# Kernel tuning notes

Hardware: AMD Instinct MI355X
Metric: run time of the kernel (lower is better)

Reference implementation:

```python
import jax, jax.numpy as jnp
import numpy as np

EMB = 2048
HD = 64            # head_dim
NH = 32            # n_heads
NKV = 8            # n_kv_groups
GS = NH // NKV     # group_size = 4
WIN = 128          # sliding_window
LAYER_IDX = 0      # even -> sliding-window mask active
ROPE_BASE = 10000.0
MAX_SEQ = 4096
YARN_ORIG = 1024.0
YARN_SCALE = 4.0
YARN_BETA_FAST = 32.0
YARN_BETA_SLOW = 1.0


def _rope_tables():
    # YaRN-adjusted RoPE tables, shape [MAX_SEQ, HD]
    freqs = 1.0 / ROPE_BASE ** (np.arange(0, HD, 2, dtype=np.float32) / HD)
    wave_len = 2.0 * np.pi / freqs
    low = YARN_ORIG / YARN_BETA_FAST
    high = YARN_ORIG / YARN_BETA_SLOW
    t = np.clip((wave_len - low) / (high - low), 0.0, 1.0)
    eff = freqs * (1.0 - t) + (freqs / YARN_SCALE) * t
    conc = 0.1 * np.log(YARN_SCALE) + 1.0
    ang = (np.arange(MAX_SEQ, dtype=np.float32)[:, None] * eff[None, :]) * conc
    ang = np.concatenate([ang, ang], axis=-1).astype(np.float32)
    return jnp.sin(ang), jnp.cos(ang)


def _apply_rope(x, sin, cos):
    # x: [B, H, S, D]; sin/cos: [B, S, D] -> broadcast over heads
    sin = sin[:, None, :, :]
    cos = cos[:, None, :, :]
    x1 = x[..., : HD // 2]
    x2 = x[..., HD // 2 :]
    rotated = jnp.concatenate([-x2, x1], axis=-1)
    return x * cos + rotated * sin


def setup_inputs() -> dict:
    key = jax.random.key(0)
    ks = jax.random.split(key, 8)
    B, S = 2, 2048
    s = 0.02
    x = jax.random.normal(ks[0], (B, S, EMB), dtype=jnp.float32)
    Wq = jax.random.normal(ks[1], (NH * HD, EMB), dtype=jnp.float32) * s
    Wk = jax.random.normal(ks[2], (NKV * HD, EMB), dtype=jnp.float32) * s
    Wv = jax.random.normal(ks[3], (NKV * HD, EMB), dtype=jnp.float32) * s
    Wo = jax.random.normal(ks[4], (EMB, NH * HD), dtype=jnp.float32) * s
    bq = jnp.zeros((NH * HD,), dtype=jnp.float32)
    bk = jnp.zeros((NKV * HD,), dtype=jnp.float32)
    bv = jnp.zeros((NKV * HD,), dtype=jnp.float32)
    bo = jnp.zeros((EMB,), dtype=jnp.float32)
    sinks = jax.random.normal(ks[5], (1, NH, 1, 1), dtype=jnp.float32)
    position_ids = jnp.arange(B * S, dtype=jnp.int64 if jax.config.jax_enable_x64 else jnp.int32).reshape(B, S)
    return {"x": x, "Wq": Wq, "bq": bq, "Wk": Wk, "bk": bk, "Wv": Wv, "bv": bv,
            "Wo": Wo, "bo": bo, "sinks": sinks, "position_ids": position_ids}


def reference(x, Wq, bq, Wk, bk, Wv, bv, Wo, bo, sinks, position_ids):
    B, S, _ = x.shape
    sin_t, cos_t = _rope_tables()
    sin = sin_t[position_ids]  # [B, S, HD]
    cos = cos_t[position_ids]

    Q = (x @ Wq.T + bq).reshape(B, S, NH, HD).transpose(0, 2, 1, 3)    # [B,NH,S,D]
    K = (x @ Wk.T + bk).reshape(B, S, NKV, HD).transpose(0, 2, 1, 3)   # [B,NKV,S,D]
    V = (x @ Wv.T + bv).reshape(B, S, NKV, HD).transpose(0, 2, 1, 3)

    Q = _apply_rope(Q, sin, cos)
    K = _apply_rope(K, sin, cos)

    # GQA without materializing repeated K/V: group query heads by kv group
    Qg = Q.reshape(B, NKV, GS, S, HD)
    scores = jnp.einsum('bgqsd,bgtd->bgqst', Qg, K) / np.sqrt(HD).astype(np.float32)

    i = jnp.arange(S)[:, None]
    j = jnp.arange(S)[None, :]
    allowed = (j <= i) & (j > i - WIN)
    scores = jnp.where(allowed, scores, -jnp.inf)

    # attention-sink logit prepended before softmax, then dropped
    sink = jnp.broadcast_to(sinks.reshape(1, NKV, GS, 1, 1), (B, NKV, GS, S, 1))
    full = jnp.concatenate([sink, scores], axis=-1)
    attn = jax.nn.softmax(full, axis=-1)[..., 1:]

    ctx = jnp.einsum('bgqst,bgtd->bgqsd', attn, V)
    ctx = ctx.reshape(B, NH, S, HD).transpose(0, 2, 1, 3).reshape(B, S, NH * HD)
    out = ctx @ Wo.T + bo
    return out
```

## Files before the change

kernel.cpp:

```cpp
#include <hip/hip_runtime.h>

typedef unsigned short u16;
typedef __bf16 bf16x8 __attribute__((ext_vector_type(8)));
typedef float f32x4 __attribute__((ext_vector_type(4)));
typedef unsigned short us8 __attribute__((ext_vector_type(8)));

__device__ inline u16 f2bf(float f) {
    union { float f; unsigned u; } v; v.f = f;
    unsigned r = v.u + 0x7FFFu + ((v.u >> 16) & 1u);
    return (u16)(r >> 16);
}
__device__ inline float bf2f(u16 h) {
    union { unsigned u; float f; } v; v.u = ((unsigned)h) << 16;
    return v.f;
}
__device__ inline f32x4 mfma16(bf16x8 a, bf16x8 b, f32x4 c) {
    return __builtin_amdgcn_mfma_f32_16x16x32_bf16(a, b, c, 0, 0, 0);
}
__device__ inline void gload_lds16(const u16* g, u16* l) {
    __builtin_amdgcn_global_load_lds(
        (const __attribute__((address_space(1))) void*)g,
        (__attribute__((address_space(3))) void*)l, 16, 0, 0);
}
union frag_cast { us8 u; bf16x8 b; };

__global__ __launch_bounds__(256)
void pack_all(const float* __restrict__ x,  const float* __restrict__ Wq,
              const float* __restrict__ Wk, const float* __restrict__ Wv,
              const float* __restrict__ Wo, const float* __restrict__ bq,
              const float* __restrict__ bk, const float* __restrict__ bv,
              u16* __restrict__ xb, u16* __restrict__ Wqkvb,
              u16* __restrict__ Wob, float* __restrict__ bqkv,
              float2* __restrict__ tab)
{
    int blk = blockIdx.x;
    if (blk >= 9217) {
        int idx = (blk - 9217) * 256 + threadIdx.x;
        int d = idx & 31, pos = idx >> 5;
        float ex = (float)d * (1.0f / 32.0f);
        float freq = powf(10000.0f, -ex);
        float wl = 6.2831853071795864f / freq;
        float tt = fminf(fmaxf((wl - 32.0f) * (1.0f / 992.0f), 0.0f), 1.0f);
        float eff = (freq * (1.0f - tt) + 0.25f * freq * tt) * 1.1386294361119891f;
        float ang = (float)pos * eff;
        tab[idx] = make_float2(cosf(ang), sinf(ang));
        return;
    }
    if (blk == 9216) {
        for (int k = threadIdx.x; k < 3072; k += 256) {
            float v;
            if (k < 2048) v = bq[k];
            else if (k < 2560) v = bk[k - 2048];
            else v = bv[k - 2560];
            bqkv[k] = v;
        }
        return;
    }
    const float* src; u16* dst; size_t off;
    if (blk < 4096)      { src = x;  dst = xb;                 off = (size_t)blk * 2048; }
    else if (blk < 6144) { src = Wq; dst = Wqkvb;              off = (size_t)(blk - 4096) * 2048; }
    else if (blk < 6656) { src = Wk; dst = Wqkvb + 4194304;    off = (size_t)(blk - 6144) * 2048; }
    else if (blk < 7168) { src = Wv; dst = Wqkvb + 5242880;    off = (size_t)(blk - 6656) * 2048; }
    else                 { src = Wo; dst = Wob;                off = (size_t)(blk - 7168) * 2048; }
    size_t i = off + (size_t)threadIdx.x * 8;
    float4 v0 = *(const float4*)(src + i);
    float4 v1 = *(const float4*)(src + i + 4);
    us8 w;
    w[0] = f2bf(v0.x); w[1] = f2bf(v0.y); w[2] = f2bf(v0.z); w[3] = f2bf(v0.w);
    w[4] = f2bf(v1.x); w[5] = f2bf(v1.y); w[6] = f2bf(v1.z); w[7] = f2bf(v1.w);
    *(us8*)(dst + i) = w;
}

template<int WNF, int OUT_BF16>
__global__ __launch_bounds__(512, 2)
void gemm_ph(const u16* __restrict__ A, const u16* __restrict__ B,
             const float* __restrict__ bias, void* __restrict__ Yv,
             int M, int N, int K)
{
    constexpr int BN = 32 * WNF;
    constexpr int BSL = BN * 32;
    constexpr int ABUF = 16384;
    constexpr int BUFU = ABUF + 2 * BSL;
    constexpr int NH2 = WNF / 2;
    __shared__ u16 lds[2 * BUFU];

    const int tid = threadIdx.x;
    const int lane = tid & 63;
    const int w = tid >> 6;
    const int wr = w >> 1, wc = w & 1;
    const int wg = blockIdx.x;
    const int swz = (wg & 7) * 32 + (wg >> 3);
    const int by = swz >> 4, bx = swz & 15;
    const long m0 = (long)by * 256;
    const long n0 = (long)bx * BN;
    const int cc = lane & 15, qq = lane >> 4;
    const int csw = (qq ^ ((cc >> 1) & 3)) << 3;

    const int sr = lane >> 2;
    const int colsw = ((lane & 3) ^ ((lane >> 3) & 3)) << 3;
    const u16* Ag = A + (m0 + sr) * (long)K + colsw;
    const u16* Bg = B + (n0 + sr) * (long)K + colsw;

    const int NT = K >> 6;

    auto STAGE = [&](int u) {
        u16* buf = &lds[(u & 1) * BUFU];
        const long k0 = (long)u * 64;
        gload_lds16(Ag + (size_t)(w * 16) * K + k0,       buf + (w * 16) * 32);
        gload_lds16(Ag + (size_t)(128 + w * 16) * K + k0, buf + (128 + w * 16) * 32);
        gload_lds16(Bg + (size_t)(w * 16) * K + k0,       buf + ABUF + (w * 16) * 32);
        if (WNF == 6) {
            if (w < 4)
                gload_lds16(Bg + (size_t)(128 + w * 16) * K + k0,
                            buf + ABUF + (128 + w * 16) * 32);
            else
                gload_lds16(Bg + (size_t)((w - 4) * 16) * K + k0 + 32,
                            buf + ABUF + BSL + ((w - 4) * 16) * 32);
        }
        gload_lds16(Ag + (size_t)(w * 16) * K + k0 + 32,       buf + 8192 + (w * 16) * 32);
        gload_lds16(Ag + (size_t)(128 + w * 16) * K + k0 + 32, buf + 8192 + (128 + w * 16) * 32);
        if (WNF == 6)
            gload_lds16(Bg + (size_t)((w + 4) * 16) * K + k0 + 32,
                        buf + ABUF + BSL + ((w + 4) * 16) * 32);
        else
            gload_lds16(Bg + (size_t)(w * 16) * K + k0 + 32,
                        buf + ABUF + BSL + (w * 16) * 32);
    };

    f32x4 acc[4][WNF];
#pragma unroll
    for (int m = 0; m < 4; ++m)
#pragma unroll
        for (int n = 0; n < WNF; ++n) acc[m][n] = (f32x4){0.f, 0.f, 0.f, 0.f};

    STAGE(0);

    for (int t = 0; t < NT; ++t) {
        const u16* buf = &lds[(t & 1) * BUFU];
        const u16* Ab0 = buf;
        const u16* Ab1 = buf + 8192;
        const u16* Bb0 = buf + ABUF;
        const u16* Bb1 = buf + ABUF + BSL;

        asm volatile("s_waitcnt vmcnt(0)" ::: "memory");
        __builtin_amdgcn_s_barrier();
        __builtin_amdgcn_sched_barrier(0);
        if (t + 1 < NT) STAGE(t + 1);
        __builtin_amdgcn_sched_barrier(0);

        bf16x8 a0[4], a1[4], bA[NH2], bB[NH2], bC[NH2], bD[NH2];

#pragma unroll
        for (int m = 0; m < 4; ++m)
            a0[m] = *(const bf16x8*)&Ab0[(wr * 64 + m * 16 + cc) * 32 + csw];
#pragma unroll
        for (int n = 0; n < NH2; ++n)
            bA[n] = *(const bf16x8*)&Bb0[(wc * (16 * WNF) + n * 16 + cc) * 32 + csw];
#pragma unroll
        for (int n = 0; n < NH2; ++n)
            bB[n] = *(const bf16x8*)&Bb0[(wc * (16 * WNF) + (NH2 + n) * 16 + cc) * 32 + csw];
        __builtin_amdgcn_sched_barrier(0);

        __builtin_amdgcn_s_setprio(1);
#pragma unroll
        for (int m = 0; m < 4; ++m)
#pragma unroll
            for (int n = 0; n < NH2; ++n)
                acc[m][n] = mfma16(a0[m], bA[n], acc[m][n]);
        __builtin_amdgcn_s_setprio(0);
        __builtin_amdgcn_sched_barrier(0);

#pragma unroll
        for (int m = 0; m < 4; ++m)
            a1[m] = *(const bf16x8*)&Ab1[(wr * 64 + m * 16 + cc) * 32 + csw];
#pragma unroll
        for (int n = 0; n < NH2; ++n)
            bC[n] = *(const bf16x8*)&Bb1[(wc * (16 * WNF) + n * 16 + cc) * 32 + csw];
        __builtin_amdgcn_sched_barrier(0);

        __builtin_amdgcn_s_setprio(1);
#pragma unroll
        for (int m = 0; m < 4; ++m)
#pragma unroll
            for (int n = 0; n < NH2; ++n)
                acc[m][NH2 + n] = mfma16(a0[m], bB[n], acc[m][NH2 + n]);
        __builtin_amdgcn_s_setprio(0);
        __builtin_amdgcn_sched_barrier(0);

#pragma unroll
        for (int n = 0; n < NH2; ++n)
            bD[n] = *(const bf16x8*)&Bb1[(wc * (16 * WNF) + (NH2 + n) * 16 + cc) * 32 + csw];
        __builtin_amdgcn_sched_barrier(0);

        __builtin_amdgcn_s_setprio(1);
#pragma unroll
        for (int m = 0; m < 4; ++m)
#pragma unroll
            for (int n = 0; n < NH2; ++n)
                acc[m][n] = mfma16(a1[m], bC[n], acc[m][n]);
        __builtin_amdgcn_s_setprio(0);
        __builtin_amdgcn_sched_barrier(0);

        __builtin_amdgcn_s_setprio(1);
#pragma unroll
        for (int m = 0; m < 4; ++m)
#pragma unroll
            for (int n = 0; n < NH2; ++n)
                acc[m][NH2 + n] = mfma16(a1[m], bD[n], acc[m][NH2 + n]);
        __builtin_amdgcn_s_setprio(0);
        __builtin_amdgcn_sched_barrier(0);
    }

#pragma unroll
    for (int m = 0; m < 4; ++m) {
#pragma unroll
        for (int n = 0; n < WNF; ++n) {
            long row = m0 + wr * 64 + m * 16 + qq * 4;
            long col = n0 + wc * (16 * WNF) + n * 16 + cc;
            float bvv = bias[col];
#pragma unroll
            for (int r2 = 0; r2 < 4; ++r2) {
                float v = acc[m][n][r2] + bvv;
                if (OUT_BF16)
                    ((u16*)Yv)[(row + r2) * (long)N + col] = f2bf(v);
                else
                    ((float*)Yv)[(row + r2) * (long)N + col] = v;
            }
        }
    }
}

__global__ __launch_bounds__(256)
void v_transpose(const u16* __restrict__ Vt, u16* __restrict__ VbT)
{
    __shared__ u16 tile[64][66];
    int s0 = blockIdx.x * 64;
    int bkv = blockIdx.y;
    int b = bkv >> 3, kv = bkv & 7;
    int t = threadIdx.x;
#pragma unroll
    for (int it = 0; it < 16; ++it) {
        int idx = t + it * 256;
        int s = idx >> 6, d = idx & 63;
        tile[s][d] = Vt[((size_t)(b * 2048 + s0 + s)) * 3072 + 2560 + kv * 64 + d];
    }
    __syncthreads();
#pragma unroll
    for (int it = 0; it < 16; ++it) {
        int idx = t + it * 256;
        int d = idx >> 6, s = idx & 63;
        VbT[((size_t)(bkv * 64 + d)) * 2048 + s0 + s] = tile[s][d];
    }
}

__global__ __launch_bounds__(256, 2)
void attn_win2(const u16* __restrict__ QKVr, const u16* __restrict__ VbT,
               const float2* __restrict__ tab, const int* __restrict__ pid,
               const float* __restrict__ sinks, u16* __restrict__ Ctx)
{
    __shared__ u16 Ks[192 * 72];
    __shared__ u16 Vs[64 * 200];
    __shared__ u16 Pb[4 * 16 * 200];
    const int S = 2048;
    const int tid = threadIdx.x;
    const int lane = tid & 63;
    const int w = tid >> 6;
    const int cc = lane & 15, qq = lane >> 4;
    const int blk = blockIdx.x;
    const int qt = blk & 31;
    const int bkv = blk >> 5;
    const int b = bkv >> 3, kv = bkv & 7;
    const int q0 = qt * 64;
    const int ks0 = q0 - 128;
    const int h = kv * 4 + w;

    {
        const int kcol = 2048 + kv * 64;
#pragma unroll
        for (int it = 0; it < 3; ++it) {
            int c = tid + it * 256;
            int kk = c >> 2, dlo = (c & 3) << 3;
            int sk = ks0 + kk;
            us8 lo = {0, 0, 0, 0, 0, 0, 0, 0};
            us8 hi = {0, 0, 0, 0, 0, 0, 0, 0};
            if (sk >= 0) {
                size_t rowoff = (size_t)(b * S + sk) * 3072 + kcol;
                us8 li = *(const us8*)(QKVr + rowoff + dlo);
                us8 hiQ = *(const us8*)(QKVr + rowoff + dlo + 32);
                int pos = pid[b * S + sk];
                const float2* tp = tab + pos * 32 + dlo;
#pragma unroll
                for (int jj = 0; jj < 8; ++jj) {
                    float2 cs = tp[jj];
                    float x1 = bf2f(li[jj]), x2 = bf2f(hiQ[jj]);
                    lo[jj] = f2bf(x1 * cs.x - x2 * cs.y);
                    hi[jj] = f2bf(x2 * cs.x + x1 * cs.y);
                }
            }
            *(us8*)&Ks[kk * 72 + dlo] = lo;
            *(us8*)&Ks[kk * 72 + dlo + 32] = hi;
        }
    }
    const u16* VtBase = VbT + (size_t)bkv * 64 * S;
#pragma unroll
    for (int it = 0; it < 6; ++it) {
        int c = tid + it * 256;
        int d = c / 24, kc = c % 24;
        int kk0 = kc << 3;
        int sk = ks0 + kk0;
        us8 v = {0, 0, 0, 0, 0, 0, 0, 0};
        if (sk >= 0) v = *(const us8*)(VtBase + (size_t)d * S + sk);
        *(us8*)&Vs[d * 200 + kk0] = v;
    }
    __syncthreads();

    const float sinkv = sinks[h];
    u16* Pw = &Pb[w * 3200];

    for (int i = 0; i < 4; ++i) {
        int m = b * S + q0 + i * 16 + cc;
        const u16* Qrow = QKVr + (size_t)m * 3072 + h * 64;
        us8 qlo = *(const us8*)(Qrow + qq * 8);
        us8 qhi = *(const us8*)(Qrow + 32 + qq * 8);
        int pos = pid[m];
        const float2* tp = tab + pos * 32 + qq * 8;
        frag_cast a0, a1;
#pragma unroll
        for (int jj = 0; jj < 8; ++jj) {
            float2 cs = tp[jj];
            float x1 = bf2f(qlo[jj]), x2 = bf2f(qhi[jj]);
            a0.u[jj] = f2bf(x1 * cs.x - x2 * cs.y);
            a1.u[jj] = f2bf(x2 * cs.x + x1 * cs.y);
        }
        bf16x8 aq0 = a0.b, aq1 = a1.b;

        f32x4 sc[12];
#pragma unroll
        for (int j = 0; j < 12; j++) sc[j] = (f32x4){0.f, 0.f, 0.f, 0.f};
#pragma unroll
        for (int j = 0; j < 12; j++) {
            bf16x8 b0 = *(const bf16x8*)&Ks[(j * 16 + cc) * 72 + qq * 8];
            bf16x8 b1 = *(const bf16x8*)&Ks[(j * 16 + cc) * 72 + 32 + qq * 8];
            sc[j] = mfma16(aq0, b0, sc[j]);
            sc[j] = mfma16(aq1, b1, sc[j]);
        }

#pragma unroll
        for (int r = 0; r < 4; ++r) {
            int qi = i * 16 + qq * 4 + r;
            float sval[12];
            float mx = -3.0e38f;
#pragma unroll
            for (int j = 0; j < 12; j++) {
                int kk = j * 16 + cc;
                float s = sc[j][r] * 0.125f;
                bool ok = (kk > qi) && (kk <= qi + 128) && (ks0 + kk >= 0);
                s = ok ? s : -3.0e38f;
                sval[j] = s;
                mx = fmaxf(mx, s);
            }
#pragma unroll
            for (int off = 1; off < 16; off <<= 1) mx = fmaxf(mx, __shfl_xor(mx, off));
            mx = fmaxf(mx, sinkv);
            float sum = 0.f;
#pragma unroll
            for (int j = 0; j < 12; j++) {
                float p = __expf(sval[j] - mx);
                sval[j] = p;
                sum += p;
            }
#pragma unroll
            for (int off = 1; off < 16; off <<= 1) sum += __shfl_xor(sum, off);
            float rden = 1.0f / (sum + __expf(sinkv - mx));
#pragma unroll
            for (int j = 0; j < 12; j++)
                Pw[(qq * 4 + r) * 200 + j * 16 + cc] = f2bf(sval[j] * rden);
        }

        f32x4 o[4];
#pragma unroll
        for (int jt = 0; jt < 4; jt++) o[jt] = (f32x4){0.f, 0.f, 0.f, 0.f};
#pragma unroll
        for (int ks = 0; ks < 6; ks++) {
            bf16x8 ap = *(const bf16x8*)&Pw[cc * 200 + ks * 32 + qq * 8];
#pragma unroll
            for (int jt = 0; jt < 4; jt++) {
                bf16x8 bv = *(const bf16x8*)&Vs[(jt * 16 + cc) * 200 + ks * 32 + qq * 8];
                o[jt] = mfma16(ap, bv, o[jt]);
            }
        }
#pragma unroll
        for (int jt = 0; jt < 4; jt++) {
#pragma unroll
            for (int r = 0; r < 4; r++) {
                size_t off = ((size_t)(b * S + q0 + i * 16 + qq * 4 + r)) * 2048
                           + h * 64 + jt * 16 + cc;
                Ctx[off] = f2bf(o[jt][r]);
            }
        }
    }
}

extern "C" void kernel_launch(void* const* d_in, const int* in_sizes, int n_in,
                              void* d_out, int out_size, void* d_ws, size_t ws_size,
                              hipStream_t stream)
{
    const float* x    = (const float*)d_in[0];
    const float* Wq   = (const float*)d_in[1];
    const float* bq   = (const float*)d_in[2];
    const float* Wk   = (const float*)d_in[3];
    const float* bk   = (const float*)d_in[4];
    const float* Wv   = (const float*)d_in[5];
    const float* bv   = (const float*)d_in[6];
    const float* Wo   = (const float*)d_in[7];
    const float* bo   = (const float*)d_in[8];
    const float* sinks = (const float*)d_in[9];
    const int*   pid  = (const int*)d_in[10];
    float* out = (float*)d_out;

    char*  ws    = (char*)d_ws;
    u16*   Wqkvb = (u16*)ws;
    u16*   Wob   = (u16*)(ws + 12582912);
    u16*   xb    = (u16*)(ws + 20971520);
    u16*   Ctx   = xb;
    u16*   QKVr  = (u16*)(ws + 37748736);
    u16*   VbT   = (u16*)(ws + 62914560);
    float* bqkv  = (float*)(ws + 67108864);
    float2* tab  = (float2*)(ws + 67121152);

    pack_all<<<9729, 256, 0, stream>>>(x, Wq, Wk, Wv, Wo, bq, bk, bv,
                                       xb, Wqkvb, Wob, bqkv, tab);

    gemm_ph<6, 1><<<256, 512, 0, stream>>>(xb, Wqkvb, bqkv, QKVr,
                                           4096, 3072, 2048);

    v_transpose<<<dim3(32, 16), 256, 0, stream>>>(QKVr, VbT);

    attn_win2<<<512, 256, 0, stream>>>(QKVr, VbT, tab, pid, sinks, Ctx);

    gemm_ph<4, 0><<<256, 512, 0, stream>>>(Ctx, Wob, bo, out,
                                           4096, 2048, 2048);
}
```

Baseline: 254.6 us.

## Split GEMM K-tile prefetch into two half-stages interleaved with MFMA phases

Restructures the bf16 GEMM main loop into a four-phase ping-pong schedule. Global-to-LDS loads for the next K tile are issued as two halves (k 0-31 and k 32-63), each placed between MFMA phases, and fine-grained vmcnt waits let compute on one half proceed while the other half is still arriving. This is meant to hide global load latency that the single full-tile wait at the top of each iteration exposed. In exchange it adds more workgroup barriers per iteration and relies on hand-counted vmcnt values, which differ per template instantiation and are fragile.

```diff
diff --git a/kernel.cpp b/kernel.cpp
--- a/kernel.cpp
+++ b/kernel.cpp
@@ -71,9 +71,9 @@
     *(us8*)(dst + i) = w;
 }
 
-template<int WNF, int OUT_BF16>
+template<int WNF, int S0V, int OUT_BF16>
 __global__ __launch_bounds__(512, 2)
-void gemm_ph(const u16* __restrict__ A, const u16* __restrict__ B,
+void gemm_p4(const u16* __restrict__ A, const u16* __restrict__ B,
              const float* __restrict__ bias, void* __restrict__ Yv,
              int M, int N, int K)
 {
@@ -81,7 +81,7 @@
     constexpr int BSL = BN * 32;
     constexpr int ABUF = 16384;
     constexpr int BUFU = ABUF + 2 * BSL;
-    constexpr int NH2 = WNF / 2;
+    constexpr int NH = WNF / 2;
     __shared__ u16 lds[2 * BUFU];
 
     const int tid = threadIdx.x;
@@ -103,7 +103,7 @@
 
     const int NT = K >> 6;
 
-    auto STAGE = [&](int u) {
+    auto STAGE0 = [&](int u) {
         u16* buf = &lds[(u & 1) * BUFU];
         const long k0 = (long)u * 64;
         gload_lds16(Ag + (size_t)(w * 16) * K + k0,       buf + (w * 16) * 32);
@@ -117,13 +117,17 @@
                 gload_lds16(Bg + (size_t)((w - 4) * 16) * K + k0 + 32,
                             buf + ABUF + BSL + ((w - 4) * 16) * 32);
         }
-        gload_lds16(Ag + (size_t)(w * 16) * K + k0 + 32,       buf + 8192 + (w * 16) * 32);
-        gload_lds16(Ag + (size_t)(128 + w * 16) * K + k0 + 32, buf + 8192 + (128 + w * 16) * 32);
+    };
+    auto STAGE1 = [&](int u) {
+        u16* buf = &lds[(u & 1) * BUFU];
+        const long k0 = (long)u * 64 + 32;
+        gload_lds16(Ag + (size_t)(w * 16) * K + k0,       buf + 8192 + (w * 16) * 32);
+        gload_lds16(Ag + (size_t)(128 + w * 16) * K + k0, buf + 8192 + (128 + w * 16) * 32);
         if (WNF == 6)
-            gload_lds16(Bg + (size_t)((w + 4) * 16) * K + k0 + 32,
+            gload_lds16(Bg + (size_t)((w + 4) * 16) * K + k0,
                         buf + ABUF + BSL + ((w + 4) * 16) * 32);
         else
-            gload_lds16(Bg + (size_t)(w * 16) * K + k0 + 32,
+            gload_lds16(Bg + (size_t)(w * 16) * K + k0,
                         buf + ABUF + BSL + (w * 16) * 32);
     };
 
@@ -133,7 +137,11 @@
 #pragma unroll
         for (int n = 0; n < WNF; ++n) acc[m][n] = (f32x4){0.f, 0.f, 0.f, 0.f};
 
-    STAGE(0);
+    STAGE0(0);
+    STAGE1(0);
+    asm volatile("s_waitcnt vmcnt(3)" ::: "memory");
+    __builtin_amdgcn_s_barrier();
+    __builtin_amdgcn_sched_barrier(0);
 
     for (int t = 0; t < NT; ++t) {
         const u16* buf = &lds[(t & 1) * BUFU];
@@ -141,73 +149,84 @@
         const u16* Ab1 = buf + 8192;
         const u16* Bb0 = buf + ABUF;
         const u16* Bb1 = buf + ABUF + BSL;
-
-        asm volatile("s_waitcnt vmcnt(0)" ::: "memory");
-        __builtin_amdgcn_s_barrier();
-        __builtin_amdgcn_sched_barrier(0);
-        if (t + 1 < NT) STAGE(t + 1);
-        __builtin_amdgcn_sched_barrier(0);
-
-        bf16x8 a0[4], a1[4], bA[NH2], bB[NH2], bC[NH2], bD[NH2];
-
-#pragma unroll
-        for (int m = 0; m < 4; ++m)
-            a0[m] = *(const bf16x8*)&Ab0[(wr * 64 + m * 16 + cc) * 32 + csw];
-#pragma unroll
-        for (int n = 0; n < NH2; ++n)
-            bA[n] = *(const bf16x8*)&Bb0[(wc * (16 * WNF) + n * 16 + cc) * 32 + csw];
-#pragma unroll
-        for (int n = 0; n < NH2; ++n)
-            bB[n] = *(const bf16x8*)&Bb0[(wc * (16 * WNF) + (NH2 + n) * 16 + cc) * 32 + csw];
-        __builtin_amdgcn_sched_barrier(0);
-
+        bf16x8 a[4], b0[NH], b1[NH];
+
+#pragma unroll
+        for (int m = 0; m < 4; ++m)
+            a[m] = *(const bf16x8*)&Ab0[(wr * 64 + m * 16 + cc) * 32 + csw];
+#pragma unroll
+        for (int n = 0; n < NH; ++n)
+            b0[n] = *(const bf16x8*)&Bb0[(wc * (16 * WNF) + n * 16 + cc) * 32 + csw];
+        __builtin_amdgcn_s_barrier();
+        asm volatile("s_waitcnt lgkmcnt(0)" ::: "memory");
+        __builtin_amdgcn_sched_barrier(0);
         __builtin_amdgcn_s_setprio(1);
 #pragma unroll
         for (int m = 0; m < 4; ++m)
 #pragma unroll
-            for (int n = 0; n < NH2; ++n)
-                acc[m][n] = mfma16(a0[m], bA[n], acc[m][n]);
+            for (int n = 0; n < NH; ++n)
+                acc[m][n] = mfma16(a[m], b0[n], acc[m][n]);
         __builtin_amdgcn_s_setprio(0);
-        __builtin_amdgcn_sched_barrier(0);
-
-#pragma unroll
-        for (int m = 0; m < 4; ++m)
-            a1[m] = *(const bf16x8*)&Ab1[(wr * 64 + m * 16 + cc) * 32 + csw];
-#pragma unroll
-        for (int n = 0; n < NH2; ++n)
-            bC[n] = *(const bf16x8*)&Bb1[(wc * (16 * WNF) + n * 16 + cc) * 32 + csw];
-        __builtin_amdgcn_sched_barrier(0);
-
+        __builtin_amdgcn_s_barrier();
+
+#pragma unroll
+        for (int n = 0; n < NH; ++n)
+            b1[n] = *(const bf16x8*)&Bb0[(wc * (16 * WNF) + (NH + n) * 16 + cc) * 32 + csw];
+        if (t + 1 < NT) STAGE0(t + 1);
+        __builtin_amdgcn_s_barrier();
+        asm volatile("s_waitcnt lgkmcnt(0)" ::: "memory");
+        __builtin_amdgcn_sched_barrier(0);
         __builtin_amdgcn_s_setprio(1);
 #pragma unroll
         for (int m = 0; m < 4; ++m)
 #pragma unroll
-            for (int n = 0; n < NH2; ++n)
-                acc[m][NH2 + n] = mfma16(a0[m], bB[n], acc[m][NH2 + n]);
+            for (int n = 0; n < NH; ++n)
+                acc[m][NH + n] = mfma16(a[m], b1[n], acc[m][NH + n]);
         __builtin_amdgcn_s_setprio(0);
-        __builtin_amdgcn_sched_barrier(0);
-
-#pragma unroll
-        for (int n = 0; n < NH2; ++n)
-            bD[n] = *(const bf16x8*)&Bb1[(wc * (16 * WNF) + (NH2 + n) * 16 + cc) * 32 + csw];
-        __builtin_amdgcn_sched_barrier(0);
-
+        if (t + 1 < NT) {
+            if constexpr (S0V == 4) asm volatile("s_waitcnt vmcnt(4)" ::: "memory");
+            else                    asm volatile("s_waitcnt vmcnt(3)" ::: "memory");
+        } else {
+            asm volatile("s_waitcnt vmcnt(0)" ::: "memory");
+        }
+        __builtin_amdgcn_s_barrier();
+        __builtin_amdgcn_sched_barrier(0);
+
+#pragma unroll
+        for (int m = 0; m < 4; ++m)
+            a[m] = *(const bf16x8*)&Ab1[(wr * 64 + m * 16 + cc) * 32 + csw];
+#pragma unroll
+        for (int n = 0; n < NH; ++n)
+            b0[n] = *(const bf16x8*)&Bb1[(wc * (16 * WNF) + n * 16 + cc) * 32 + csw];
+        __builtin_amdgcn_s_barrier();
+        asm volatile("s_waitcnt lgkmcnt(0)" ::: "memory");
+        __builtin_amdgcn_sched_barrier(0);
         __builtin_amdgcn_s_setprio(1);
 #pragma unroll
         for (int m = 0; m < 4; ++m)
 #pragma unroll
-            for (int n = 0; n < NH2; ++n)
-                acc[m][n] = mfma16(a1[m], bC[n], acc[m][n]);
+            for (int n = 0; n < NH; ++n)
+                acc[m][n] = mfma16(a[m], b0[n], acc[m][n]);
         __builtin_amdgcn_s_setprio(0);
-        __builtin_amdgcn_sched_barrier(0);
-
+        __builtin_amdgcn_s_barrier();
+
+#pragma unroll
+        for (int n = 0; n < NH; ++n)
+            b1[n] = *(const bf16x8*)&Bb1[(wc * (16 * WNF) + (NH + n) * 16 + cc) * 32 + csw];
+        if (t + 1 < NT) STAGE1(t + 1);
+        __builtin_amdgcn_s_barrier();
+        asm volatile("s_waitcnt lgkmcnt(0)" ::: "memory");
+        __builtin_amdgcn_sched_barrier(0);
         __builtin_amdgcn_s_setprio(1);
 #pragma unroll
         for (int m = 0; m < 4; ++m)
 #pragma unroll
-            for (int n = 0; n < NH2; ++n)
-                acc[m][NH2 + n] = mfma16(a1[m], bD[n], acc[m][NH2 + n]);
+            for (int n = 0; n < NH; ++n)
+                acc[m][NH + n] = mfma16(a[m], b1[n], acc[m][NH + n]);
         __builtin_amdgcn_s_setprio(0);
+        if (t + 1 < NT) asm volatile("s_waitcnt vmcnt(3)" ::: "memory");
+        else            asm volatile("s_waitcnt vmcnt(0)" ::: "memory");
+        __builtin_amdgcn_s_barrier();
         __builtin_amdgcn_sched_barrier(0);
     }
 
@@ -431,13 +450,13 @@
     pack_all<<<9729, 256, 0, stream>>>(x, Wq, Wk, Wv, Wo, bq, bk, bv,
                                        xb, Wqkvb, Wob, bqkv, tab);
 
-    gemm_ph<6, 1><<<256, 512, 0, stream>>>(xb, Wqkvb, bqkv, QKVr,
-                                           4096, 3072, 2048);
+    gemm_p4<6, 4, 1><<<256, 512, 0, stream>>>(xb, Wqkvb, bqkv, QKVr,
+                                              4096, 3072, 2048);
 
     v_transpose<<<dim3(32, 16), 256, 0, stream>>>(QKVr, VbT);
 
     attn_win2<<<512, 256, 0, stream>>>(QKVr, VbT, tab, pid, sinks, Ctx);
 
-    gemm_ph<4, 0><<<256, 512, 0, stream>>>(Ctx, Wob, bo, out,
-                                           4096, 2048, 2048);
-}
+    gemm_p4<4, 3, 0><<<256, 512, 0, stream>>>(Ctx, Wob, bo, out,
+                                              4096, 2048, 2048);
+}
```

After: 256.6 us. No clear change (+0.8%).
